# Kernel tuning notes

Measured on AMD Instinct MI355X. Metric: run time of the kernel, lower is better.

The kernel has to match this reference:

```python
import jax, jax.numpy as jnp
import numpy as np
import math

B, T, E = 1, 2048, 2048
H, D = 16, 128
L = 64
RA_WINDOW = 64
RA_ALPHA = 0.5


def setup_inputs() -> dict:
    key = jax.random.key(0)
    ks = jax.random.split(key, 7)
    s_e = 1.0 / math.sqrt(E)
    s_l = 1.0 / math.sqrt(L)
    return {
        "hidden_states": jax.random.normal(ks[0], (B, T, E), jnp.float32),
        "Wq": jax.random.normal(ks[1], (E, E), jnp.float32) * s_e,       # q_proj.weight [out,in]
        "Wk": jax.random.normal(ks[2], (L, E), jnp.float32) * s_e,       # k_down.weight
        "Wv": jax.random.normal(ks[3], (L, E), jnp.float32) * s_e,       # v_down.weight
        "q_to_latent": jax.random.normal(ks[4], (H, D, L), jnp.float32) * (1.0 / math.sqrt(D)),
        "v_up": jax.random.normal(ks[5], (H, L, D), jnp.float32) * s_l,
        "Wo": jax.random.normal(ks[6], (E, E), jnp.float32) * s_e,       # out_proj.weight
    }


def reference(hidden_states, Wq, Wk, Wv, q_to_latent, v_up, Wo):
    B_, T_, E_ = hidden_states.shape
    NEG = jnp.asarray(-1e30, hidden_states.dtype)

    # per-head queries [B,T,H,D]
    Q = (hidden_states @ Wq.T).reshape(B_, T_, H, D)
    # shared latent K/V [B,T,L]
    latent_k = hidden_states @ Wk.T
    latent_v = hidden_states @ Wv.T

    # per-head Q -> latent alignment [B,T,H,L]
    q_latent = jnp.einsum('bthd,hdl->bthl', Q, q_to_latent)

    inv_sqrt_L = 1.0 / math.sqrt(L)
    # main latent-compressed logits [B,H,T,T]
    logits = jnp.einsum('bthl,bsl->bhts', q_latent, latent_k) * inv_sqrt_L

    i = jnp.arange(T_)[:, None]
    j = jnp.arange(T_)[None, :]
    causal = j <= i                       # [T,T]
    logits = jnp.where(causal[None, None], logits, NEG)

    # reciprocal band pass. NOTE: einsum labels (d vs l) intentionally mismatch,
    # faithfully reproducing the source's outer-product-of-sums computation.
    logits_recip = jnp.einsum('bthd,bsl->bhts', q_latent, latent_k) * inv_sqrt_L
    band = (jnp.abs(i - j) <= RA_WINDOW) & causal
    logits = jnp.where(band[None, None], logits + RA_ALPHA * logits_recip, logits)

    attn = jax.nn.softmax(logits, axis=-1)  # [B,H,T,T]

    # per-head V up-projection [B,T,H,D]
    V_exp = jnp.einsum('btl,hld->bthd', latent_v, v_up)
    ctx = jnp.einsum('bhts,bshd->bthd', attn, V_exp)
    out = ctx.reshape(B_, T_, H * D) @ Wo.T
    return out
```

## Files before the change

### kernel.cpp

```cpp
#include <hip/hip_runtime.h>


#define T_ 2048
#define E_ 2048
#define H_ 16
#define D_ 128
#define L_ 64
#define NQ 1152

typedef float  floatx4 __attribute__((ext_vector_type(4)));
typedef __bf16 bf16x8  __attribute__((ext_vector_type(8)));

__device__ __forceinline__ ushort f2b(float x){
  unsigned int u = __float_as_uint(x);
  u = (u + 0x7fffu + ((u >> 16) & 1u)) >> 16;
  return (ushort)u;
}
__device__ __forceinline__ float blo(unsigned int u){ return __uint_as_float(u << 16); }
__device__ __forceinline__ float bhi(unsigned int u){ return __uint_as_float(u & 0xffff0000u); }

__device__ __forceinline__ void glds16(const ushort* g, ushort* l){
#if __has_builtin(__builtin_amdgcn_global_load_lds)
  __builtin_amdgcn_global_load_lds((const __attribute__((address_space(1))) void*)g,
                                   (__attribute__((address_space(3))) void*)l, 16, 0, 0);
#else
  *(uint4*)l = *(const uint4*)g;
#endif
}

__global__ __launch_bounds__(256)
void k_f2b4(const float* __restrict__ a, ushort* __restrict__ oa,
            const float* __restrict__ b, ushort* __restrict__ ob,
            const float* __restrict__ c, ushort* __restrict__ oc,
            const float* __restrict__ d, ushort* __restrict__ od){
  int bid = blockIdx.x; const float* src; ushort* dst; int base;
  if (bid < 4096){ src=a; dst=oa; base=bid; }
  else if (bid < 8192){ src=b; dst=ob; base=bid-4096; }
  else if (bid < 8320){ src=c; dst=oc; base=bid-8192; }
  else { src=d; dst=od; base=bid-8320; }
  int i = (base*256 + (int)threadIdx.x)*4;
  float4 v = *(const float4*)(src + i);
  ushort4 o; o.x=f2b(v.x); o.y=f2b(v.y); o.z=f2b(v.z); o.w=f2b(v.w);
  *(ushort4*)(dst + i) = o;
}

__global__ __launch_bounds__(128)
void k_prep_wql(const float* __restrict__ Wq, const float* __restrict__ q2l,
                ushort* __restrict__ Wql){
  const int h = blockIdx.z, lh = blockIdx.y;
  const int e = blockIdx.x*128 + threadIdx.x;
  const float* qb = q2l + (size_t)h*D_*L_ + lh*32;
  float acc[32];
  #pragma unroll
  for (int i=0;i<32;++i) acc[i]=0.f;
  for (int d=0; d<128; ++d){
    float wv = Wq[(size_t)(h*128+d)*E_ + e];
    #pragma unroll
    for (int i=0;i<32;++i) acc[i] += wv*qb[(size_t)d*64 + i];
  }
  #pragma unroll
  for (int i=0;i<32;++i) Wql[(size_t)(h*64 + lh*32 + i)*E_ + e] = f2b(acc[i]);
}

__global__ __launch_bounds__(256)
void k_prep_vupT(const float* __restrict__ vup, ushort* __restrict__ vupT){
  const int h = blockIdx.x, tid = threadIdx.x;
  for (int idx = tid; idx < L_*D_; idx += 256){
    int l = idx >> 7, d = idx & 127;
    vupT[(size_t)h*D_*L_ + d*64 + l] = f2b(vup[(size_t)h*L_*D_ + idx]);
  }
}

template<int MT,int NT,bool OB16>
__global__ __launch_bounds__(256)
void gemm_glds2(const ushort* __restrict__ A, const ushort* __restrict__ B,
                float* __restrict__ Cf, ushort* __restrict__ Cb,
                int M, int N, int K, float scale){
  constexpr int BM = 32*MT, BN = 32*NT;
  constexpr int IA = BM/32, IB = BN/32;
  __shared__ ushort As[BM*64];
  __shared__ ushort Bs[BN*64];
  const int tid = threadIdx.x, lane = tid&63, wv = tid>>6;
  const int wm = wv & 1, wn = wv >> 1;
  const int l15 = lane&15, quad = lane>>4;
  const int nbx = (int)gridDim.x, nwg = nbx*(int)gridDim.y;
  int bid = (int)blockIdx.y*nbx + (int)blockIdx.x;
  bid = (bid & 7)*(nwg >> 3) + (bid >> 3);
  const int m0 = (bid / nbx)*BM, n0 = (bid % nbx)*BN;
  const float sc = (n0 < 1024) ? scale : 1.0f;
  floatx4 acc[MT][NT] = {};
  for (int k0=0; k0<K; k0+=64){
    __syncthreads();
    #pragma unroll
    for (int j=0;j<IA;++j){
      int cc = j*256 + tid; int row = cc>>3, kc = ((cc&7)^(row&7))*8;
      glds16(A + (size_t)(m0+row)*K + k0 + kc, &As[cc*8]);
    }
    #pragma unroll
    for (int j=0;j<IB;++j){
      int cc = j*256 + tid; int row = cc>>3, kc = ((cc&7)^(row&7))*8;
      glds16(B + (size_t)(n0+row)*K + k0 + kc, &Bs[cc*8]);
    }
    __syncthreads();
    #pragma unroll
    for (int kk=0;kk<2;++kk){
      bf16x8 af[MT], bfr[NT];
      #pragma unroll
      for (int mi=0;mi<MT;++mi){
        const int r = wm*MT*16 + mi*16 + l15;
        af[mi] = *(const bf16x8*)(&As[r*64 + (((kk*4+quad)^(r&7))<<3)]);
      }
      #pragma unroll
      for (int ni=0;ni<NT;++ni){
        const int r = wn*NT*16 + ni*16 + l15;
        bfr[ni] = *(const bf16x8*)(&Bs[r*64 + (((kk*4+quad)^(r&7))<<3)]);
      }
      #pragma unroll
      for (int mi=0;mi<MT;++mi)
        #pragma unroll
        for (int ni=0;ni<NT;++ni)
          acc[mi][ni] = __builtin_amdgcn_mfma_f32_16x16x32_bf16(af[mi], bfr[ni], acc[mi][ni], 0,0,0);
    }
  }
  #pragma unroll
  for (int mi=0;mi<MT;++mi){
    const int rb = m0 + wm*MT*16 + mi*16 + quad*4;
    #pragma unroll
    for (int ni=0;ni<NT;++ni){
      const int col = n0 + wn*NT*16 + ni*16 + l15;
      #pragma unroll
      for (int r=0;r<4;++r){
        if constexpr (OB16) Cb[(size_t)(rb+r)*N + col] = f2b(acc[mi][ni][r]*sc);
        else                Cf[(size_t)(rb+r)*N + col] = acc[mi][ni][r];
      }
    }
  }
}

__global__ __launch_bounds__(256)
void k_rowsums(const ushort* __restrict__ qkvb,
               float* __restrict__ rsq, float* __restrict__ rsk){
  int i = blockIdx.x*256 + threadIdx.x;
  const ushort* src; float* dst;
  if (i < T_*H_){
    int t = i>>4, g = i&15;
    src = qkvb + (size_t)t*NQ + g*64; dst = rsq + i;
  } else {
    int t = i - T_*H_;
    if (t >= T_) return;
    src = qkvb + (size_t)t*NQ + 1024; dst = rsk + t;
  }
  const uint4* p = (const uint4*)src;
  float s = 0.f;
  #pragma unroll
  for (int j=0;j<8;++j){
    uint4 u = p[j];
    const unsigned int uu[4] = {u.x,u.y,u.z,u.w};
    #pragma unroll
    for (int q=0;q<4;++q){ s += blo(uu[q]); s += bhi(uu[q]); }
  }
  *dst = s;
}

__global__ __launch_bounds__(256)
void k_vexp_mfma(const ushort* __restrict__ qkvb, const ushort* __restrict__ vupT,
                 ushort* __restrict__ vexpT){
  const int h = blockIdx.y, t0 = blockIdx.x*64;
  const int tid = threadIdx.x, lane = tid&63, w = tid>>6;
  const int l15 = lane&15, quad = lane>>4;
  bf16x8 a[2][2], b[4][2];
  #pragma unroll
  for (int mt=0;mt<2;++mt)
    #pragma unroll
    for (int kk=0;kk<2;++kk)
      a[mt][kk] = *(const bf16x8*)(vupT + (size_t)h*D_*L_ + (w*32+mt*16+l15)*64 + kk*32 + quad*8);
  #pragma unroll
  for (int nt=0;nt<4;++nt)
    #pragma unroll
    for (int kk=0;kk<2;++kk)
      b[nt][kk] = *(const bf16x8*)(qkvb + (size_t)(t0+nt*16+l15)*NQ + 1088 + kk*32 + quad*8);
  floatx4 acc[2][4] = {};
  #pragma unroll
  for (int mt=0;mt<2;++mt)
    #pragma unroll
    for (int nt=0;nt<4;++nt)
      #pragma unroll
      for (int kk=0;kk<2;++kk)
        acc[mt][nt] = __builtin_amdgcn_mfma_f32_16x16x32_bf16(a[mt][kk], b[nt][kk], acc[mt][nt], 0,0,0);
  #pragma unroll
  for (int mt=0;mt<2;++mt)
    #pragma unroll
    for (int nt=0;nt<4;++nt)
      #pragma unroll
      for (int r=0;r<4;++r)
        vexpT[((size_t)h*D_ + w*32+mt*16+quad*4+r)*T_ + t0 + nt*16 + l15] = f2b(acc[mt][nt][r]);
}

__global__ __launch_bounds__(256, 4)
void k_attn(const ushort* __restrict__ qkvb,
            const float*  __restrict__ rsq,
            const float*  __restrict__ rsk,
            const ushort* __restrict__ vexpT,
            ushort*       __restrict__ ctx,
            ushort*       __restrict__ partO,
            float*        __restrict__ partML,
            int CH){
  __shared__ ushort Ks[64*64];
  __shared__ ushort Vts[128*64];
  __shared__ ushort Ps[4*16*64];
  const int h  = blockIdx.y;
  const int bxr = (int)gridDim.x - 1 - (int)blockIdx.x;
  int qt, c;
  if (CH == 8){
    if (bxr < 8){ qt = bxr; c = 0; }
    else if (bxr < 24){ int u = bxr-8;  qt = 8  + (u>>1); c = u&1; }
    else if (bxr < 48){ int u = bxr-24; qt = 16 + u/3;    c = u - (u/3)*3; }
    else               { int u = bxr-48; qt = 24 + (u>>2); c = u&3; }
  } else { qt = bxr; c = 0; }
  const int nct = (qt + CH) / CH;
  const int stBeg = c*CH, stEnd = min(qt, stBeg + CH - 1);
  const int t0 = qt*64;
  const int tid = threadIdx.x, lane = tid & 63, w = tid >> 6;
  const int l15 = lane & 15, quad = lane >> 4;

  auto stageK = [&](int s0k){
    #pragma unroll
    for (int j=0;j<2;++j){ int cc = tid + j*256;
      int row = cc>>3, kc = ((cc&7) ^ (row&7))*8;
      glds16(qkvb + (size_t)(s0k + row)*NQ + 1024 + kc, &Ks[cc*8]); }
  };
  auto stageV = [&](int s0v){
    #pragma unroll
    for (int j=0;j<4;++j){ int cc = tid + j*256;
      int row = cc>>3, sc2 = ((cc&7) ^ (row&7))*8;
      glds16(vexpT + ((size_t)h*128 + row)*T_ + s0v + sc2, &Vts[cc*8]); }
  };

  const int qrow = t0 + w*16 + l15;
  const bf16x8 q0 = *(const bf16x8*)(qkvb + (size_t)qrow*NQ + h*64 + quad*8);
  const bf16x8 q1 = *(const bf16x8*)(qkvb + (size_t)qrow*NQ + h*64 + 32 + quad*8);
  const float rqv = rsq[(size_t)qrow*H_ + h] * 0.5f;

  float mrun = -INFINITY, lrun = 0.f;
  floatx4 o[8] = {};

  stageK(stBeg*64); stageV(stBeg*64);

  for (int st=stBeg; st<=stEnd; ++st){
    const int s0 = st*64;
    const bool more = (st < stEnd);
    asm volatile("s_waitcnt vmcnt(4)" ::: "memory");
    __builtin_amdgcn_s_barrier();
    __builtin_amdgcn_sched_barrier(0);
    floatx4 sT[4] = {};
    __builtin_amdgcn_s_setprio(1);
    #pragma unroll
    for (int jt=0;jt<4;++jt){
      const int srow = jt*16 + l15, sx = srow & 7;
      bf16x8 k0f = *(const bf16x8*)(&Ks[srow*64 + (quad^sx)*8]);
      sT[jt] = __builtin_amdgcn_mfma_f32_16x16x32_bf16(k0f, q0, sT[jt], 0,0,0);
      bf16x8 k1f = *(const bf16x8*)(&Ks[srow*64 + ((4+quad)^sx)*8]);
      sT[jt] = __builtin_amdgcn_mfma_f32_16x16x32_bf16(k1f, q1, sT[jt], 0,0,0);
    }
    __builtin_amdgcn_s_setprio(0);
    __builtin_amdgcn_sched_barrier(0);
    __builtin_amdgcn_s_barrier();
    if (more) stageK(s0 + 64);
    float mloc = -3.0e38f;
    if (st >= qt-1){
      #pragma unroll
      for (int jt=0;jt<4;++jt){
        const float4 rk4 = *(const float4*)(rsk + s0 + jt*16 + quad*4);
        #pragma unroll
        for (int r=0;r<4;++r){
          const int sg = s0 + jt*16 + quad*4 + r;
          const int dd = qrow - sg;
          float x = sT[jt][r];
          x = (dd <= 64) ? x + rqv*((const float*)&rk4)[r] : x;
          x = (dd < 0)   ? -3.0e38f : x;
          sT[jt][r] = x; mloc = fmaxf(mloc, x);
        }
      }
    } else {
      #pragma unroll
      for (int jt=0;jt<4;++jt)
        #pragma unroll
        for (int r=0;r<4;++r) mloc = fmaxf(mloc, sT[jt][r]);
    }
    mloc = fmaxf(mloc, __shfl_xor(mloc, 16));
    mloc = fmaxf(mloc, __shfl_xor(mloc, 32));
    const float mn = (mloc - mrun <= 6.0f) ? mrun : mloc;
    const float al = exp2f(mrun - mn);
    float ss = 0.f;
    #pragma unroll
    for (int jt=0;jt<4;++jt)
      #pragma unroll
      for (int r=0;r<4;++r){
        float p = exp2f(sT[jt][r]-mn); sT[jt][r] = p; ss += p;
      }
    ss += __shfl_xor(ss, 16); ss += __shfl_xor(ss, 32);
    lrun = lrun*al + ss; mrun = mn;
    #pragma unroll
    for (int jt=0;jt<4;++jt){
      unsigned p01, p23;
      asm volatile("v_cvt_pk_bf16_f32 %0, %1, %2" : "=v"(p01) : "v"(sT[jt][0]), "v"(sT[jt][1]));
      asm volatile("v_cvt_pk_bf16_f32 %0, %1, %2" : "=v"(p23) : "v"(sT[jt][2]), "v"(sT[jt][3]));
      const int chunk = 2*jt + (quad>>1);
      uint2 pw2; pw2.x = p01; pw2.y = p23;
      *(uint2*)(&Ps[(w*16 + l15)*64 + ((chunk ^ (l15&7))<<3) + (quad&1)*4]) = pw2;
    }
    if (__any(al < 1.0f)){
      float alr[4];
      #pragma unroll
      for (int r=0;r<4;++r) alr[r] = __shfl(al, quad*4 + r);
      #pragma unroll
      for (int nt=0;nt<8;++nt){
        o[nt][0]*=alr[0]; o[nt][1]*=alr[1]; o[nt][2]*=alr[2]; o[nt][3]*=alr[3];
      }
    }
    __builtin_amdgcn_sched_barrier(0);
    if (more) asm volatile("s_waitcnt vmcnt(2)" ::: "memory");
    else      asm volatile("s_waitcnt vmcnt(0)" ::: "memory");
    __builtin_amdgcn_s_barrier();
    __builtin_amdgcn_sched_barrier(0);
    __builtin_amdgcn_s_setprio(1);
    #pragma unroll
    for (int kks=0;kks<2;++kks){
      const int ch = kks*4 + quad;
      bf16x8 pf = *(const bf16x8*)(&Ps[(w*16 + l15)*64 + ((ch ^ (l15&7))<<3)]);
      #pragma unroll
      for (int nt=0;nt<8;++nt){
        const int vrow = nt*16 + l15, vx = vrow & 7;
        bf16x8 vf = *(const bf16x8*)(&Vts[vrow*64 + ((kks*4+quad)^vx)*8]);
        o[nt] = __builtin_amdgcn_mfma_f32_16x16x32_bf16(pf, vf, o[nt], 0,0,0);
      }
    }
    __builtin_amdgcn_s_setprio(0);
    __builtin_amdgcn_sched_barrier(0);
    if (more){
      __builtin_amdgcn_s_barrier();
      stageV(s0 + 64);
    }
  }
  const float linv = 1.f/lrun;
  float lr4[4];
  #pragma unroll
  for (int r=0;r<4;++r) lr4[r] = __shfl(linv, quad*4 + r);
  if (nct == 1){
    #pragma unroll
    for (int r=0;r<4;++r){
      const int row = t0 + w*16 + quad*4 + r;
      #pragma unroll
      for (int nt=0;nt<8;++nt)
        ctx[(size_t)row*E_ + h*D_ + nt*16 + l15] = f2b(o[nt][r]*lr4[r]);
    }
  } else {
    const int slot = (h*24 + (qt-8))*4 + c;
    ushort* po = partO + (size_t)slot*8192;
    #pragma unroll
    for (int nt=0;nt<8;++nt)
      #pragma unroll
      for (int r=0;r<4;++r)
        po[((w*8+nt)*4+r)*64 + quad*16 + l15] = f2b(o[nt][r]*lr4[r]);
    if (quad == 0){
      float2 ml; ml.x = mrun; ml.y = lrun;
      ((float2*)partML)[(size_t)slot*64 + w*16 + l15] = ml;
    }
  }
}

__global__ __launch_bounds__(256)
void k_merge(const ushort* __restrict__ partO, const float* __restrict__ partML,
             ushort* __restrict__ ctx){
  const int h = blockIdx.y, qt = 8 + blockIdx.x;
  const int nct = (qt + 8) / 8;
  const int tid = threadIdx.x;
  const int rg = tid >> 2, d0 = (tid & 3)*32;
  const int w = rg >> 4, quad = (rg >> 2) & 3, rr = rg & 3;
  const int n0 = d0 >> 4;
  const int sbase = (h*24 + (qt-8))*4;
  float m[4], l[4], M = -INFINITY;
  for (int c=0;c<4;++c){
    if (c < nct){
      float2 v = ((const float2*)partML)[(size_t)(sbase+c)*64 + rg];
      m[c]=v.x; l[c]=v.y; M = fmaxf(M, v.x);
    }
  }
  float lt = 0.f, wgt[4];
  for (int c=0;c<4;++c){
    if (c < nct){ wgt[c] = exp2f(m[c]-M)*l[c]; lt += wgt[c]; }
  }
  const float inv = 1.f/lt;
  float acc[32];
  #pragma unroll
  for (int i=0;i<32;++i) acc[i]=0.f;
  for (int c=0;c<4;++c){
    if (c >= nct) break;
    const float sc = wgt[c]*inv;
    const ushort* po = partO + (size_t)(sbase+c)*8192;
    #pragma unroll
    for (int nn=0;nn<2;++nn){
      const ushort* p2 = po + ((w*8 + n0+nn)*4 + rr)*64 + quad*16;
      uint4 u  = *(const uint4*)p2;
      uint4 u2 = *(const uint4*)(p2 + 8);
      const unsigned int uu[8] = {u.x,u.y,u.z,u.w,u2.x,u2.y,u2.z,u2.w};
      #pragma unroll
      for (int q=0;q<8;++q){
        acc[nn*16+q*2]   += sc*blo(uu[q]);
        acc[nn*16+q*2+1] += sc*bhi(uu[q]);
      }
    }
  }
  ushort* dst = ctx + (size_t)(qt*64 + rg)*E_ + h*D_ + d0;
  #pragma unroll
  for (int k=0;k<8;++k){
    ushort4 ov; ov.x=f2b(acc[k*4]); ov.y=f2b(acc[k*4+1]);
    ov.z=f2b(acc[k*4+2]); ov.w=f2b(acc[k*4+3]);
    *(ushort4*)(dst + k*4) = ov;
  }
}

extern "C" void kernel_launch(void* const* d_in, const int* in_sizes, int n_in,
                              void* d_out, int out_size, void* d_ws, size_t ws_size,
                              hipStream_t stream) {
  const float* hs  = (const float*)d_in[0];
  const float* Wq  = (const float*)d_in[1];
  const float* Wk  = (const float*)d_in[2];
  const float* Wv  = (const float*)d_in[3];
  const float* q2l = (const float*)d_in[4];
  const float* vup = (const float*)d_in[5];
  const float* Wo  = (const float*)d_in[6];
  float* out = (float*)d_out;
  char* ws = (char*)d_ws;

  ushort* hsb   = (ushort*)(ws + 0);
  ushort* Wqkvb = (ushort*)(ws + 8388608);
  ushort* Wob   = (ushort*)(ws + 13107200);
  ushort* qkvb  = (ushort*)(ws + 21495808);
  ushort* vupT  = (ushort*)(ws + 26214400);
  float*  rsqp  = (float*) (ws + 26476544);
  float*  rskp  = (float*) (ws + 26607616);
  ushort* vexpT = (ushort*)(ws + 26615808);
  ushort* ctxb  = (ushort*)(ws + 35004416);
  ushort* partO = (ushort*)(ws + 43393024);
  float*  partML= (float*) (ws + 68558848);
  const size_t NEED = 69345280;
  const int CH = (ws_size >= NEED) ? 8 : 32;

  k_f2b4<<<8448, 256, 0, stream>>>(hs, hsb, Wo, Wob,
                                   Wk, Wqkvb + (size_t)1024*E_,
                                   Wv, Wqkvb + (size_t)1088*E_);

  k_prep_wql<<<dim3(16,2,16), 128, 0, stream>>>(Wq, q2l, Wqkvb);
  k_prep_vupT<<<16, 256, 0, stream>>>(vup, vupT);

  gemm_glds2<2,2,true><<<dim3(18,32), 256, 0, stream>>>(
      hsb, Wqkvb, nullptr, qkvb, T_, NQ, E_, 0.18033688f);

  k_rowsums<<<136, 256, 0, stream>>>(qkvb, rsqp, rskp);

  k_vexp_mfma<<<dim3(32,16), 256, 0, stream>>>(qkvb, vupT, vexpT);

  k_attn<<<dim3(CH==8 ? 80 : 32, 16), 256, 0, stream>>>(
      qkvb, rsqp, rskp, vexpT, ctxb, partO, partML, CH);

  if (CH == 8)
    k_merge<<<dim3(24,16), 256, 0, stream>>>(partO, partML, ctxb);

  gemm_glds2<2,4,false><<<dim3(16,32), 256, 0, stream>>>(
      ctxb, Wob, out, nullptr, T_, E_, E_, 1.0f);
}
```

Baseline: 254.5 us.

## Double-buffer K/V LDS tiles in attention and cut per-iteration barriers

The attention kernel now keeps two LDS buffers each for the K and V tiles. The next tile's K and V are loaded at the top of each iteration, and the current tile's band-term rsk values are also fetched early. This removes two of the four barriers and waits per key tile, so global loads can overlap both the QK and PV MFMA phases. In exchange, LDS use grows and the launch bound drops from 4 to 2 blocks per CU, which lowers occupancy and the latency hiding that more resident waves would provide.

Result: no change. 257.0 us (+1.0%).

```diff
diff --git a/kernel.cpp b/kernel.cpp
--- a/kernel.cpp
+++ b/kernel.cpp
@@ -196,7 +196,7 @@
         vexpT[((size_t)h*D_ + w*32+mt*16+quad*4+r)*T_ + t0 + nt*16 + l15] = f2b(acc[mt][nt][r]);
 }
 
-__global__ __launch_bounds__(256, 4)
+__global__ __launch_bounds__(256, 2)
 void k_attn(const ushort* __restrict__ qkvb,
             const float*  __restrict__ rsq,
             const float*  __restrict__ rsk,
@@ -205,8 +205,8 @@
             ushort*       __restrict__ partO,
             float*        __restrict__ partML,
             int CH){
-  __shared__ ushort Ks[64*64];
-  __shared__ ushort Vts[128*64];
+  __shared__ ushort Ks[2][64*64];
+  __shared__ ushort Vts[2][128*64];
   __shared__ ushort Ps[4*16*64];
   const int h  = blockIdx.y;
   const int bxr = (int)gridDim.x - 1 - (int)blockIdx.x;
@@ -223,17 +223,17 @@
   const int tid = threadIdx.x, lane = tid & 63, w = tid >> 6;
   const int l15 = lane & 15, quad = lane >> 4;
 
-  auto stageK = [&](int s0k){
+  auto stageK = [&](int b, int s0k){
     #pragma unroll
     for (int j=0;j<2;++j){ int cc = tid + j*256;
       int row = cc>>3, kc = ((cc&7) ^ (row&7))*8;
-      glds16(qkvb + (size_t)(s0k + row)*NQ + 1024 + kc, &Ks[cc*8]); }
+      glds16(qkvb + (size_t)(s0k + row)*NQ + 1024 + kc, &Ks[b][cc*8]); }
   };
-  auto stageV = [&](int s0v){
+  auto stageV = [&](int b, int s0v){
     #pragma unroll
     for (int j=0;j<4;++j){ int cc = tid + j*256;
       int row = cc>>3, sc2 = ((cc&7) ^ (row&7))*8;
-      glds16(vexpT + ((size_t)h*128 + row)*T_ + s0v + sc2, &Vts[cc*8]); }
+      glds16(vexpT + ((size_t)h*128 + row)*T_ + s0v + sc2, &Vts[b][cc*8]); }
   };
 
   const int qrow = t0 + w*16 + l15;
@@ -244,12 +244,21 @@
   float mrun = -INFINITY, lrun = 0.f;
   floatx4 o[8] = {};
 
-  stageK(stBeg*64); stageV(stBeg*64);
+  stageK(0, stBeg*64); stageV(0, stBeg*64);
 
   for (int st=stBeg; st<=stEnd; ++st){
     const int s0 = st*64;
+    const int cur = (st - stBeg) & 1;
     const bool more = (st < stEnd);
-    asm volatile("s_waitcnt vmcnt(4)" ::: "memory");
+    const bool edge = (st >= qt-1);
+    float4 rk[4];
+    if (edge){
+      #pragma unroll
+      for (int jt=0;jt<4;++jt) rk[jt] = *(const float4*)(rsk + s0 + jt*16 + quad*4);
+    }
+    if (more){ stageK(cur^1, s0 + 64); stageV(cur^1, s0 + 64); }
+    if (more) asm volatile("s_waitcnt vmcnt(6)" ::: "memory");
+    else      asm volatile("s_waitcnt vmcnt(0)" ::: "memory");
     __builtin_amdgcn_s_barrier();
     __builtin_amdgcn_sched_barrier(0);
     floatx4 sT[4] = {};
@@ -257,26 +266,22 @@
     #pragma unroll
     for (int jt=0;jt<4;++jt){
       const int srow = jt*16 + l15, sx = srow & 7;
-      bf16x8 k0f = *(const bf16x8*)(&Ks[srow*64 + (quad^sx)*8]);
+      bf16x8 k0f = *(const bf16x8*)(&Ks[cur][srow*64 + (quad^sx)*8]);
       sT[jt] = __builtin_amdgcn_mfma_f32_16x16x32_bf16(k0f, q0, sT[jt], 0,0,0);
-      bf16x8 k1f = *(const bf16x8*)(&Ks[srow*64 + ((4+quad)^sx)*8]);
+      bf16x8 k1f = *(const bf16x8*)(&Ks[cur][srow*64 + ((4+quad)^sx)*8]);
       sT[jt] = __builtin_amdgcn_mfma_f32_16x16x32_bf16(k1f, q1, sT[jt], 0,0,0);
     }
     __builtin_amdgcn_s_setprio(0);
-    __builtin_amdgcn_sched_barrier(0);
-    __builtin_amdgcn_s_barrier();
-    if (more) stageK(s0 + 64);
     float mloc = -3.0e38f;
-    if (st >= qt-1){
+    if (edge){
       #pragma unroll
       for (int jt=0;jt<4;++jt){
-        const float4 rk4 = *(const float4*)(rsk + s0 + jt*16 + quad*4);
         #pragma unroll
         for (int r=0;r<4;++r){
           const int sg = s0 + jt*16 + quad*4 + r;
           const int dd = qrow - sg;
           float x = sT[jt][r];
-          x = (dd <= 64) ? x + rqv*((const float*)&rk4)[r] : x;
+          x = (dd <= 64) ? x + rqv*((const float*)&rk[jt])[r] : x;
           x = (dd < 0)   ? -3.0e38f : x;
           sT[jt][r] = x; mloc = fmaxf(mloc, x);
         }
@@ -318,11 +323,6 @@
         o[nt][0]*=alr[0]; o[nt][1]*=alr[1]; o[nt][2]*=alr[2]; o[nt][3]*=alr[3];
       }
     }
-    __builtin_amdgcn_sched_barrier(0);
-    if (more) asm volatile("s_waitcnt vmcnt(2)" ::: "memory");
-    else      asm volatile("s_waitcnt vmcnt(0)" ::: "memory");
-    __builtin_amdgcn_s_barrier();
-    __builtin_amdgcn_sched_barrier(0);
     __builtin_amdgcn_s_setprio(1);
     #pragma unroll
     for (int kks=0;kks<2;++kks){
@@ -331,16 +331,13 @@
       #pragma unroll
       for (int nt=0;nt<8;++nt){
         const int vrow = nt*16 + l15, vx = vrow & 7;
-        bf16x8 vf = *(const bf16x8*)(&Vts[vrow*64 + ((kks*4+quad)^vx)*8]);
+        bf16x8 vf = *(const bf16x8*)(&Vts[cur][vrow*64 + ((kks*4+quad)^vx)*8]);
         o[nt] = __builtin_amdgcn_mfma_f32_16x16x32_bf16(pf, vf, o[nt], 0,0,0);
       }
     }
     __builtin_amdgcn_s_setprio(0);
     __builtin_amdgcn_sched_barrier(0);
-    if (more){
-      __builtin_amdgcn_s_barrier();
-      stageV(s0 + 64);
-    }
+    if (more) __builtin_amdgcn_s_barrier();
   }
   const float linv = 1.f/lrun;
   float lr4[4];
```
